# Kernel optimization log

Hardware: AMD Instinct MI355X
Metric: run time of the kernel (lower is better)

## Reference

```python
import jax, jax.numpy as jnp
import numpy as np

NEG_INF = -1e9  # matches masked_fill value -1000000000.0
SLOPE = 0.2     # LeakyReLU negative slope


def setup_inputs() -> dict:
    key = jax.random.key(0)
    k1, k2, k3, k4 = jax.random.split(key, 4)
    B, N, Fin, Fout = 16, 1024, 256, 256
    h = jax.random.normal(k1, (B, N, Fin), dtype=jnp.float32)
    adj = jax.random.randint(k2, (B, N, N), 0, 2, dtype=jnp.int32)
    W = jax.random.normal(k3, (Fin, Fout), dtype=jnp.float32) * (1.0 / np.sqrt(Fin))
    a = jax.random.normal(k4, (2 * Fout,), dtype=jnp.float32) * (1.0 / np.sqrt(2 * Fout))
    return {"h": h, "adj": adj, "W": W, "a": a}


def reference(h, adj, W, a):
    # h: [B,N,Fin], adj: [B,N,N] (0/1), W: [Fin,Fout], a: [2*Fout]
    Fout = W.shape[1]
    Wh = jnp.einsum("bnf,fo->bno", h, W)            # [B,N,Fout]
    a1, a2 = a[:Fout], a[Fout:]
    # e[b,i,j] = leakyrelu( Wh[b,i]·a1 + Wh[b,j]·a2 )  == a(cat(Wh_i, Wh_j))
    f1 = Wh @ a1                                     # [B,N]
    f2 = Wh @ a2                                     # [B,N]
    e = jax.nn.leaky_relu(f1[:, :, None] + f2[:, None, :], negative_slope=SLOPE)
    e = jnp.where(adj == 0, NEG_INF, e)              # mask non-edges
    attention = jax.nn.softmax(e, axis=-1)           # [B,N,N]
    # dropout is identity at eval / p=0
    h_prime = jnp.einsum("bij,bjo->bio", attention, Wh)  # [B,N,Fout]
    return h_prime
```

## Files before the change

kernel.cpp:

```cpp
#include <hip/hip_runtime.h>

typedef __attribute__((ext_vector_type(8))) short bf16x8;
typedef __attribute__((ext_vector_type(4))) float f32x4;

__device__ __forceinline__ unsigned short f2bf(float x) {
    unsigned int u = __float_as_uint(x);
    u += 0x7FFFu + ((u >> 16) & 1u);
    return (unsigned short)(u >> 16);
}

__device__ __forceinline__ void gl_lds16(const void* g, void* l) {
    __builtin_amdgcn_global_load_lds(
        (__attribute__((address_space(1))) void*)((void*)g),
        (__attribute__((address_space(3))) void*)l, 16, 0, 0);
}

__global__ __launch_bounds__(256) void prep(const float* __restrict__ W,
                                            short* __restrict__ WbT) {
    __shared__ float tile[32][33];
    const int t = threadIdx.x;
    const int bx = blockIdx.x & 7, by = blockIdx.x >> 3;
    const int r0 = by * 32, c0 = bx * 32;
    const int lr = t >> 5, lc = t & 31;
#pragma unroll
    for (int q = 0; q < 4; ++q)
        tile[q * 8 + lr][lc] = W[(r0 + q * 8 + lr) * 256 + c0 + lc];
    __syncthreads();
#pragma unroll
    for (int q = 0; q < 4; ++q)
        WbT[(c0 + q * 8 + lr) * 256 + r0 + lc] = (short)f2bf(tile[lc][q * 8 + lr]);
}

__global__ __launch_bounds__(256, 4) void wh_f12(const float* __restrict__ h,
                                                 const short* __restrict__ WbT,
                                                 const float* __restrict__ a,
                                                 short* __restrict__ WhT,
                                                 float* __restrict__ f1,
                                                 float* __restrict__ f2) {
    __shared__ short hA[32][264];
    __shared__ float sp[2][4][32];
    const int t = threadIdx.x;
    const int wid = t >> 6, lane = t & 63;
    const int quad = lane >> 4, l15 = lane & 15;
    const int m0 = blockIdx.x * 32;

#pragma unroll
    for (int rr = 0; rr < 2; ++rr) {
        const int r = rr * 16 + (t >> 4), c0 = (t & 15) * 16;
        const float* hp = h + (size_t)(m0 + r) * 256 + c0;
        float4 v0 = *(const float4*)(hp + 0), v1 = *(const float4*)(hp + 4);
        float4 v2 = *(const float4*)(hp + 8), v3 = *(const float4*)(hp + 12);
        bf16x8 w0, w1;
        w0[0] = (short)f2bf(v0.x); w0[1] = (short)f2bf(v0.y);
        w0[2] = (short)f2bf(v0.z); w0[3] = (short)f2bf(v0.w);
        w0[4] = (short)f2bf(v1.x); w0[5] = (short)f2bf(v1.y);
        w0[6] = (short)f2bf(v1.z); w0[7] = (short)f2bf(v1.w);
        w1[0] = (short)f2bf(v2.x); w1[1] = (short)f2bf(v2.y);
        w1[2] = (short)f2bf(v2.z); w1[3] = (short)f2bf(v2.w);
        w1[4] = (short)f2bf(v3.x); w1[5] = (short)f2bf(v3.y);
        w1[6] = (short)f2bf(v3.z); w1[7] = (short)f2bf(v3.w);
        *(bf16x8*)&hA[r][c0] = w0;
        *(bf16x8*)&hA[r][c0 + 8] = w1;
    }
    __syncthreads();

    f32x4 acc[2][4] = {};
#pragma unroll
    for (int kt = 0; kt < 8; ++kt) {
        const int k0 = kt * 32;
        bf16x8 bv[4];
#pragma unroll
        for (int ft = 0; ft < 4; ++ft)
            bv[ft] = *(const bf16x8*)(WbT + (size_t)(wid * 64 + ft * 16 + l15) * 256 + k0 + quad * 8);
        bf16x8 a0 = *(const bf16x8*)&hA[l15][k0 + quad * 8];
        bf16x8 a1 = *(const bf16x8*)&hA[16 + l15][k0 + quad * 8];
#pragma unroll
        for (int ft = 0; ft < 4; ++ft) {
            acc[0][ft] = __builtin_amdgcn_mfma_f32_16x16x32_bf16(a0, bv[ft], acc[0][ft], 0, 0, 0);
            acc[1][ft] = __builtin_amdgcn_mfma_f32_16x16x32_bf16(a1, bv[ft], acc[1][ft], 0, 0, 0);
        }
    }

    const int b = m0 >> 10;
#pragma unroll
    for (int mf = 0; mf < 2; ++mf) {
        const int il0 = (m0 & 1023) + mf * 16 + quad * 4;
#pragma unroll
        for (int ft = 0; ft < 4; ++ft) {
            const int f = wid * 64 + ft * 16 + l15;
            ushort4 pk;
            pk.x = f2bf(acc[mf][ft][0]);
            pk.y = f2bf(acc[mf][ft][1]);
            pk.z = f2bf(acc[mf][ft][2]);
            pk.w = f2bf(acc[mf][ft][3]);
            *(ushort4*)(WhT + ((size_t)b << 18) + (size_t)f * 1024 + il0) = pk;
        }
    }

    float a1v[4], a2v[4];
#pragma unroll
    for (int ft = 0; ft < 4; ++ft) {
        a1v[ft] = a[wid * 64 + ft * 16 + l15];
        a2v[ft] = a[256 + wid * 64 + ft * 16 + l15];
    }
    float p1[2][4] = {}, p2[2][4] = {};
#pragma unroll
    for (int mf = 0; mf < 2; ++mf)
#pragma unroll
        for (int ft = 0; ft < 4; ++ft)
#pragma unroll
            for (int r = 0; r < 4; ++r) {
                p1[mf][r] += acc[mf][ft][r] * a1v[ft];
                p2[mf][r] += acc[mf][ft][r] * a2v[ft];
            }
#pragma unroll
    for (int off = 1; off < 16; off <<= 1)
#pragma unroll
        for (int mf = 0; mf < 2; ++mf)
#pragma unroll
            for (int r = 0; r < 4; ++r) {
                p1[mf][r] += __shfl_xor(p1[mf][r], off);
                p2[mf][r] += __shfl_xor(p2[mf][r], off);
            }
    if (l15 == 0)
#pragma unroll
        for (int mf = 0; mf < 2; ++mf)
#pragma unroll
            for (int r = 0; r < 4; ++r) {
                sp[0][wid][mf * 16 + quad * 4 + r] = p1[mf][r];
                sp[1][wid][mf * 16 + quad * 4 + r] = p2[mf][r];
            }
    __syncthreads();
    if (t < 32) {
        f1[m0 + t] = sp[0][0][t] + sp[0][1][t] + sp[0][2][t] + sp[0][3][t];
        f2[m0 + t] = sp[1][0][t] + sp[1][1][t] + sp[1][2][t] + sp[1][3][t];
    }
}

__global__ __launch_bounds__(256, 2) void fused_agg(const int* __restrict__ adj,
                                                    const float* __restrict__ f1g,
                                                    const float* __restrict__ f2g,
                                                    const short* __restrict__ WhT,
                                                    float* __restrict__ out) {
    __shared__ short Ps[32 * 64];
    __shared__ short Bs[256 * 64];
    __shared__ float lred[256];
    __shared__ float linv[32];

    const int t = threadIdx.x;
    const int wid = t >> 6, lane = t & 63;
    const int quad = lane >> 4, l15 = lane & 15;

    const int id = blockIdx.x;
    const int xcd = id & 7, rest = id >> 3;
    const int b = xcd + 8 * (rest & 1);
    const int m0 = (rest >> 1) * 32;

    const int r = t >> 3, jc = t & 7;
    const float f1r = f1g[(b << 10) + m0 + r];
    const int* arow = adj + ((size_t)b << 20) + (size_t)(m0 + r) * 1024 + jc * 8;
    const float* f2p = f2g + (b << 10) + jc * 8;
    short* psw = Ps + r * 64 + (size_t)((jc ^ (r & 7)) * 8);

    const short* Wb = WhT + ((size_t)b << 18);
    const int rq0 = t >> 3, wB = (t & 7) ^ (rq0 & 7);
    const short* gB = Wb + (size_t)rq0 * 1024 + wB * 8;
    short* lB = Bs + t * 8;

    const int nq = wid * 64;
    f32x4 acc[2][4] = {};
    float lacc = 0.f;

    for (int k0 = 0; k0 < 1024; k0 += 64) {
#pragma unroll
        for (int q = 0; q < 8; ++q)
            gl_lds16(gB + k0 + q * 32768, lB + q * 2048);

        int4 a0 = *(const int4*)(arow + k0);
        int4 a1 = *(const int4*)(arow + k0 + 4);
        float4 w0 = *(const float4*)(f2p + k0);
        float4 w1 = *(const float4*)(f2p + k0 + 4);
        float xs[8] = {w0.x, w0.y, w0.z, w0.w, w1.x, w1.y, w1.z, w1.w};
        int ms[8] = {a0.x, a0.y, a0.z, a0.w, a1.x, a1.y, a1.z, a1.w};
        float pv[8];
#pragma unroll
        for (int u = 0; u < 8; ++u) {
            float x = f1r + xs[u];
            x = fmaxf(x, 0.2f * x);
            pv[u] = ms[u] ? __expf(x) : 0.f;
            lacc += pv[u];
        }
        bf16x8 pw;
#pragma unroll
        for (int u = 0; u < 8; ++u) pw[u] = (short)f2bf(pv[u]);
        *(bf16x8*)psw = pw;
        __syncthreads();

#pragma unroll
        for (int kt = 0; kt < 2; ++kt) {
            const int w = kt * 4 + quad;
            bf16x8 av[2], bv[4];
#pragma unroll
            for (int mf = 0; mf < 2; ++mf) {
                const int ra = mf * 16 + l15;
                av[mf] = *(const bf16x8*)(Ps + ra * 64 + ((w ^ (ra & 7)) * 8));
            }
#pragma unroll
            for (int nf = 0; nf < 4; ++nf) {
                const int rb = nq + nf * 16 + l15;
                bv[nf] = *(const bf16x8*)(Bs + rb * 64 + ((w ^ (rb & 7)) * 8));
            }
#pragma unroll
            for (int mf = 0; mf < 2; ++mf)
#pragma unroll
                for (int nf = 0; nf < 4; ++nf)
                    acc[mf][nf] = __builtin_amdgcn_mfma_f32_16x16x32_bf16(av[mf], bv[nf], acc[mf][nf], 0, 0, 0);
        }
        __syncthreads();
    }

    lred[t] = lacc;
    __syncthreads();
    if (t < 32) {
        const float* lp = lred + t * 8;
        linv[t] = 1.0f / (((lp[0] + lp[1]) + (lp[2] + lp[3])) +
                          ((lp[4] + lp[5]) + (lp[6] + lp[7])));
    }
    __syncthreads();

#pragma unroll
    for (int mf = 0; mf < 2; ++mf) {
        const int il = mf * 16 + quad * 4;
        const float i0 = linv[il], i1 = linv[il + 1];
        const float i2 = linv[il + 2], i3 = linv[il + 3];
#pragma unroll
        for (int nf = 0; nf < 4; ++nf) {
            float* op = out + (size_t)((b << 10) + m0 + il) * 256 + nq + nf * 16 + l15;
            op[0]   = acc[mf][nf][0] * i0;
            op[256] = acc[mf][nf][1] * i1;
            op[512] = acc[mf][nf][2] * i2;
            op[768] = acc[mf][nf][3] * i3;
        }
    }
}

extern "C" void kernel_launch(void* const* d_in, const int* in_sizes, int n_in,
                              void* d_out, int out_size, void* d_ws, size_t ws_size,
                              hipStream_t stream) {
    const float* h   = (const float*)d_in[0];
    const int*   adj = (const int*)d_in[1];
    const float* W   = (const float*)d_in[2];
    const float* a   = (const float*)d_in[3];
    float* out = (float*)d_out;

    short* WbT = (short*)d_ws;
    float* f1  = (float*)(WbT + 65536);
    float* f2  = f1 + 16384;
    short* WhT = (short*)(f2 + 16384);

    prep<<<64, 256, 0, stream>>>(W, WbT);
    wh_f12<<<512, 256, 0, stream>>>(h, WbT, a, WhT, f1, f2);
    fused_agg<<<512, 256, 0, stream>>>(adj, f1, f2, WhT, out);
}
```

Baseline: 148.0 us.

## Double-buffer LDS tiles to prefetch next adjacency and Wh tiles during MFMA

Doubles the P and B shared-memory tiles and restructures the K loop into a software pipeline. The global-to-LDS load of the next Wh tile and the adjacency/f2 loads for the next step are issued before the current MFMA block, and the next attention probabilities are computed after it. This removes one barrier per iteration and aims to hide global latency behind matrix math. In exchange LDS use roughly doubles to about 72KB per block, which may reduce how many blocks fit per CU under launch_bounds(256,2).

```diff
diff --git a/kernel.cpp b/kernel.cpp
--- a/kernel.cpp
+++ b/kernel.cpp
@@ -142,8 +142,8 @@
                                                     const float* __restrict__ f2g,
                                                     const short* __restrict__ WhT,
                                                     float* __restrict__ out) {
-    __shared__ short Ps[32 * 64];
-    __shared__ short Bs[256 * 64];
+    __shared__ short Ps[2][32 * 64];
+    __shared__ short Bs[2][256 * 64];
     __shared__ float lred[256];
     __shared__ float linv[32];
 
@@ -160,41 +160,56 @@
     const float f1r = f1g[(b << 10) + m0 + r];
     const int* arow = adj + ((size_t)b << 20) + (size_t)(m0 + r) * 1024 + jc * 8;
     const float* f2p = f2g + (b << 10) + jc * 8;
-    short* psw = Ps + r * 64 + (size_t)((jc ^ (r & 7)) * 8);
+    const int pswo = r * 64 + ((jc ^ (r & 7)) * 8);
 
     const short* Wb = WhT + ((size_t)b << 18);
     const int rq0 = t >> 3, wB = (t & 7) ^ (rq0 & 7);
     const short* gB = Wb + (size_t)rq0 * 1024 + wB * 8;
-    short* lB = Bs + t * 8;
 
     const int nq = wid * 64;
     f32x4 acc[2][4] = {};
     float lacc = 0.f;
 
-    for (int k0 = 0; k0 < 1024; k0 += 64) {
-#pragma unroll
-        for (int q = 0; q < 8; ++q)
-            gl_lds16(gB + k0 + q * 32768, lB + q * 2048);
-
-        int4 a0 = *(const int4*)(arow + k0);
-        int4 a1 = *(const int4*)(arow + k0 + 4);
-        float4 w0 = *(const float4*)(f2p + k0);
-        float4 w1 = *(const float4*)(f2p + k0 + 4);
+#pragma unroll
+    for (int q = 0; q < 8; ++q)
+        gl_lds16(gB + q * 32768, &Bs[0][0] + t * 8 + q * 2048);
+    {
+        int4 a0 = *(const int4*)(arow);
+        int4 a1 = *(const int4*)(arow + 4);
+        float4 w0 = *(const float4*)(f2p);
+        float4 w1 = *(const float4*)(f2p + 4);
         float xs[8] = {w0.x, w0.y, w0.z, w0.w, w1.x, w1.y, w1.z, w1.w};
         int ms[8] = {a0.x, a0.y, a0.z, a0.w, a1.x, a1.y, a1.z, a1.w};
-        float pv[8];
+        bf16x8 pw;
 #pragma unroll
         for (int u = 0; u < 8; ++u) {
             float x = f1r + xs[u];
             x = fmaxf(x, 0.2f * x);
-            pv[u] = ms[u] ? __expf(x) : 0.f;
-            lacc += pv[u];
-        }
-        bf16x8 pw;
-#pragma unroll
-        for (int u = 0; u < 8; ++u) pw[u] = (short)f2bf(pv[u]);
-        *(bf16x8*)psw = pw;
-        __syncthreads();
+            float pv = ms[u] ? __expf(x) : 0.f;
+            lacc += pv;
+            pw[u] = (short)f2bf(pv);
+        }
+        *(bf16x8*)(&Ps[0][0] + pswo) = pw;
+    }
+    __syncthreads();
+
+    for (int tt = 0; tt < 16; ++tt) {
+        const int cur = tt & 1;
+        const short* PsC = &Ps[cur][0];
+        const short* BsC = &Bs[cur][0];
+
+        int4 na0, na1;
+        float4 nw0, nw1;
+        if (tt < 15) {
+            const int k1 = (tt + 1) * 64;
+#pragma unroll
+            for (int q = 0; q < 8; ++q)
+                gl_lds16(gB + k1 + q * 32768, &Bs[cur ^ 1][0] + t * 8 + q * 2048);
+            na0 = *(const int4*)(arow + k1);
+            na1 = *(const int4*)(arow + k1 + 4);
+            nw0 = *(const float4*)(f2p + k1);
+            nw1 = *(const float4*)(f2p + k1 + 4);
+        }
 
 #pragma unroll
         for (int kt = 0; kt < 2; ++kt) {
@@ -203,18 +218,33 @@
 #pragma unroll
             for (int mf = 0; mf < 2; ++mf) {
                 const int ra = mf * 16 + l15;
-                av[mf] = *(const bf16x8*)(Ps + ra * 64 + ((w ^ (ra & 7)) * 8));
+                av[mf] = *(const bf16x8*)(PsC + ra * 64 + ((w ^ (ra & 7)) * 8));
             }
 #pragma unroll
             for (int nf = 0; nf < 4; ++nf) {
                 const int rb = nq + nf * 16 + l15;
-                bv[nf] = *(const bf16x8*)(Bs + rb * 64 + ((w ^ (rb & 7)) * 8));
+                bv[nf] = *(const bf16x8*)(BsC + rb * 64 + ((w ^ (rb & 7)) * 8));
             }
 #pragma unroll
             for (int mf = 0; mf < 2; ++mf)
 #pragma unroll
                 for (int nf = 0; nf < 4; ++nf)
                     acc[mf][nf] = __builtin_amdgcn_mfma_f32_16x16x32_bf16(av[mf], bv[nf], acc[mf][nf], 0, 0, 0);
+        }
+
+        if (tt < 15) {
+            float xs[8] = {nw0.x, nw0.y, nw0.z, nw0.w, nw1.x, nw1.y, nw1.z, nw1.w};
+            int ms[8] = {na0.x, na0.y, na0.z, na0.w, na1.x, na1.y, na1.z, na1.w};
+            bf16x8 pw;
+#pragma unroll
+            for (int u = 0; u < 8; ++u) {
+                float x = f1r + xs[u];
+                x = fmaxf(x, 0.2f * x);
+                float pv = ms[u] ? __expf(x) : 0.f;
+                lacc += pv;
+                pw[u] = (short)f2bf(pv);
+            }
+            *(bf16x8*)(&Ps[cur ^ 1][0] + pswo) = pw;
         }
         __syncthreads();
     }
```

Result: slower. 152.7 us (+3.2%).

## Precompute full attention row tile in LDS and stream Wh directly from global

Applied to the files above, without the earlier changes.

The aggregation kernel now uses 512-thread blocks covering 64 rows. It first computes the full 64x1024 bf16 probability tile into LDS (128KB) with a single barrier, instead of interleaving P production and Wh tile staging per 64-wide K step. Wh B-fragments are then loaded directly from global/L2 into registers with double buffering, removing the global-to-LDS staging and the per-iteration barriers. The cost is heavy LDS use, which limits occupancy to one block per CU, and more global/L2 traffic for Wh because each wave fetches its B fragments itself.

```diff
diff --git a/kernel.cpp b/kernel.cpp
--- a/kernel.cpp
+++ b/kernel.cpp
@@ -7,12 +7,6 @@
     unsigned int u = __float_as_uint(x);
     u += 0x7FFFu + ((u >> 16) & 1u);
     return (unsigned short)(u >> 16);
-}
-
-__device__ __forceinline__ void gl_lds16(const void* g, void* l) {
-    __builtin_amdgcn_global_load_lds(
-        (__attribute__((address_space(1))) void*)((void*)g),
-        (__attribute__((address_space(3))) void*)l, 16, 0, 0);
 }
 
 __global__ __launch_bounds__(256) void prep(const float* __restrict__ W,
@@ -137,15 +131,14 @@
     }
 }
 
-__global__ __launch_bounds__(256, 2) void fused_agg(const int* __restrict__ adj,
+__global__ __launch_bounds__(512, 2) void fused_agg(const int* __restrict__ adj,
                                                     const float* __restrict__ f1g,
                                                     const float* __restrict__ f2g,
                                                     const short* __restrict__ WhT,
                                                     float* __restrict__ out) {
-    __shared__ short Ps[32 * 64];
-    __shared__ short Bs[256 * 64];
-    __shared__ float lred[256];
-    __shared__ float linv[32];
+    __shared__ short Ps[64 * 1024];
+    __shared__ float lred[512];
+    __shared__ float linv[64];
 
     const int t = threadIdx.x;
     const int wid = t >> 6, lane = t & 63;
@@ -154,74 +147,85 @@
     const int id = blockIdx.x;
     const int xcd = id & 7, rest = id >> 3;
     const int b = xcd + 8 * (rest & 1);
-    const int m0 = (rest >> 1) * 32;
+    const int m0 = (rest >> 1) * 64;
 
     const int r = t >> 3, jc = t & 7;
     const float f1r = f1g[(b << 10) + m0 + r];
     const int* arow = adj + ((size_t)b << 20) + (size_t)(m0 + r) * 1024 + jc * 8;
     const float* f2p = f2g + (b << 10) + jc * 8;
-    short* psw = Ps + r * 64 + (size_t)((jc ^ (r & 7)) * 8);
-
-    const short* Wb = WhT + ((size_t)b << 18);
-    const int rq0 = t >> 3, wB = (t & 7) ^ (rq0 & 7);
-    const short* gB = Wb + (size_t)rq0 * 1024 + wB * 8;
-    short* lB = Bs + t * 8;
-
-    const int nq = wid * 64;
-    f32x4 acc[2][4] = {};
+    short* prow = Ps + r * 1024;
+    const int rx = r & 7;
     float lacc = 0.f;
-
-    for (int k0 = 0; k0 < 1024; k0 += 64) {
-#pragma unroll
-        for (int q = 0; q < 8; ++q)
-            gl_lds16(gB + k0 + q * 32768, lB + q * 2048);
-
-        int4 a0 = *(const int4*)(arow + k0);
-        int4 a1 = *(const int4*)(arow + k0 + 4);
-        float4 w0 = *(const float4*)(f2p + k0);
-        float4 w1 = *(const float4*)(f2p + k0 + 4);
+#pragma unroll 4
+    for (int i = 0; i < 16; ++i) {
+        int4 a0 = *(const int4*)(arow + i * 64);
+        int4 a1 = *(const int4*)(arow + i * 64 + 4);
+        float4 w0 = *(const float4*)(f2p + i * 64);
+        float4 w1 = *(const float4*)(f2p + i * 64 + 4);
         float xs[8] = {w0.x, w0.y, w0.z, w0.w, w1.x, w1.y, w1.z, w1.w};
         int ms[8] = {a0.x, a0.y, a0.z, a0.w, a1.x, a1.y, a1.z, a1.w};
-        float pv[8];
+        bf16x8 pw;
 #pragma unroll
         for (int u = 0; u < 8; ++u) {
             float x = f1r + xs[u];
             x = fmaxf(x, 0.2f * x);
-            pv[u] = ms[u] ? __expf(x) : 0.f;
-            lacc += pv[u];
-        }
-        bf16x8 pw;
-#pragma unroll
-        for (int u = 0; u < 8; ++u) pw[u] = (short)f2bf(pv[u]);
-        *(bf16x8*)psw = pw;
-        __syncthreads();
-
+            float pv = ms[u] ? __expf(x) : 0.f;
+            lacc += pv;
+            pw[u] = (short)f2bf(pv);
+        }
+        *(bf16x8*)(prow + (((i * 8 + jc) ^ rx) * 8)) = pw;
+    }
+    lred[t] = lacc;
+    __syncthreads();
+
+    const int wm = wid >> 2, wn = wid & 3;
+    const int mh = wm * 32, nq = wn * 64;
+    const short* Wb = WhT + ((size_t)b << 18);
+    const short* pB0 = Wb + (size_t)(nq + l15) * 1024 + quad * 8;
+    const short* pB1 = pB0 + 16 * 1024;
+    const short* pB2 = pB0 + 32 * 1024;
+    const short* pB3 = pB0 + 48 * 1024;
+    const short* rowA0 = Ps + (size_t)(mh + l15) * 1024;
+    const short* rowA1 = rowA0 + 16 * 1024;
+    const int sx = l15 & 7;
+
+    f32x4 acc[2][4] = {};
+    bf16x8 bA[8], bB[8];
+
+    auto loadB = [&](bf16x8* dst, int T) {
 #pragma unroll
         for (int kt = 0; kt < 2; ++kt) {
-            const int w = kt * 4 + quad;
-            bf16x8 av[2], bv[4];
-#pragma unroll
-            for (int mf = 0; mf < 2; ++mf) {
-                const int ra = mf * 16 + l15;
-                av[mf] = *(const bf16x8*)(Ps + ra * 64 + ((w ^ (ra & 7)) * 8));
-            }
+            dst[kt * 4 + 0] = *(const bf16x8*)(pB0 + T * 64 + kt * 32);
+            dst[kt * 4 + 1] = *(const bf16x8*)(pB1 + T * 64 + kt * 32);
+            dst[kt * 4 + 2] = *(const bf16x8*)(pB2 + T * 64 + kt * 32);
+            dst[kt * 4 + 3] = *(const bf16x8*)(pB3 + T * 64 + kt * 32);
+        }
+    };
+    auto tile = [&](bf16x8* bv, int T) {
+#pragma unroll
+        for (int kt = 0; kt < 2; ++kt) {
+            const int sw = ((T * 8 + kt * 4 + quad) ^ sx) * 8;
+            bf16x8 av0 = *(const bf16x8*)(rowA0 + sw);
+            bf16x8 av1 = *(const bf16x8*)(rowA1 + sw);
 #pragma unroll
             for (int nf = 0; nf < 4; ++nf) {
-                const int rb = nq + nf * 16 + l15;
-                bv[nf] = *(const bf16x8*)(Bs + rb * 64 + ((w ^ (rb & 7)) * 8));
-            }
-#pragma unroll
-            for (int mf = 0; mf < 2; ++mf)
-#pragma unroll
-                for (int nf = 0; nf < 4; ++nf)
-                    acc[mf][nf] = __builtin_amdgcn_mfma_f32_16x16x32_bf16(av[mf], bv[nf], acc[mf][nf], 0, 0, 0);
-        }
-        __syncthreads();
-    }
-
-    lred[t] = lacc;
-    __syncthreads();
-    if (t < 32) {
+                acc[0][nf] = __builtin_amdgcn_mfma_f32_16x16x32_bf16(av0, bv[kt * 4 + nf], acc[0][nf], 0, 0, 0);
+                acc[1][nf] = __builtin_amdgcn_mfma_f32_16x16x32_bf16(av1, bv[kt * 4 + nf], acc[1][nf], 0, 0, 0);
+            }
+        }
+    };
+
+    loadB(bA, 0);
+#pragma unroll
+    for (int tp = 0; tp < 8; ++tp) {
+        const int t0 = tp * 2, t1 = t0 + 1;
+        loadB(bB, t1);
+        tile(bA, t0);
+        if (t1 < 15) loadB(bA, t1 + 1);
+        tile(bB, t1);
+    }
+
+    if (t < 64) {
         const float* lp = lred + t * 8;
         linv[t] = 1.0f / (((lp[0] + lp[1]) + (lp[2] + lp[3])) +
                           ((lp[4] + lp[5]) + (lp[6] + lp[7])));
@@ -230,7 +234,7 @@
 
 #pragma unroll
     for (int mf = 0; mf < 2; ++mf) {
-        const int il = mf * 16 + quad * 4;
+        const int il = mh + mf * 16 + quad * 4;
         const float i0 = linv[il], i1 = linv[il + 1];
         const float i2 = linv[il + 2], i3 = linv[il + 3];
 #pragma unroll
@@ -260,5 +264,5 @@
 
     prep<<<64, 256, 0, stream>>>(W, WbT);
     wh_f12<<<512, 256, 0, stream>>>(h, WbT, a, WhT, f1, f2);
-    fused_agg<<<512, 256, 0, stream>>>(adj, f1, f2, WhT, out);
-}
+    fused_agg<<<256, 512, 0, stream>>>(adj, f1, f2, WhT, out);
+}
```

Result: slower. 154.5 us (+4.4%).

## Bitpack adjacency, enlarge agg tiles, and triple-buffer WhT staging

Applied to the files above, without the earlier changes.

Adds a separate kernel that packs the int32 adjacency mask into 64-bit bitmasks with wave ballots. The aggregation kernel then reads the bits from LDS instead of streaming int32 adjacency. The aggregation kernel now uses 512-thread blocks covering 64 rows each, halving redundant WhT loads per output row. It also triple-buffers the WhT tiles and double-buffers the P tiles, with explicit waitcnt and barriers so loads and P generation overlap the MFMAs. The extra bitpack pass still reads all of adj once, and the larger LDS footprint may limit occupancy.

```diff
diff --git a/kernel.cpp b/kernel.cpp
--- a/kernel.cpp
+++ b/kernel.cpp
@@ -14,6 +14,8 @@
         (__attribute__((address_space(1))) void*)((void*)g),
         (__attribute__((address_space(3))) void*)l, 16, 0, 0);
 }
+
+#define SFENCE __builtin_amdgcn_sched_barrier(0)
 
 __global__ __launch_bounds__(256) void prep(const float* __restrict__ W,
                                             short* __restrict__ WbT) {
@@ -29,6 +31,21 @@
 #pragma unroll
     for (int q = 0; q < 4; ++q)
         WbT[(c0 + q * 8 + lr) * 256 + r0 + lc] = (short)f2bf(tile[lc][q * 8 + lr]);
+}
+
+__global__ __launch_bounds__(256) void bitpack(const int* __restrict__ adj,
+                                               unsigned long long* __restrict__ bits) {
+    const int wid = threadIdx.x >> 6, lane = threadIdx.x & 63;
+    const int row = blockIdx.x * 4 + wid;
+    const int* arow = adj + (size_t)row * 1024;
+    unsigned long long myword = 0ull;
+#pragma unroll
+    for (int w = 0; w < 16; ++w) {
+        int v = arow[w * 64 + lane];
+        unsigned long long bal = __ballot(v != 0);
+        if (lane == w) myword = bal;
+    }
+    if (lane < 16) bits[(size_t)row * 16 + lane] = myword;
 }
 
 __global__ __launch_bounds__(256, 4) void wh_f12(const float* __restrict__ h,
@@ -137,15 +154,17 @@
     }
 }
 
-__global__ __launch_bounds__(256, 2) void fused_agg(const int* __restrict__ adj,
+__global__ __launch_bounds__(512, 2) void fused_agg(const unsigned long long* __restrict__ bitsG,
                                                     const float* __restrict__ f1g,
                                                     const float* __restrict__ f2g,
                                                     const short* __restrict__ WhT,
                                                     float* __restrict__ out) {
-    __shared__ short Ps[32 * 64];
-    __shared__ short Bs[256 * 64];
-    __shared__ float lred[256];
-    __shared__ float linv[32];
+    __shared__ short Bs[3][256 * 64];
+    __shared__ short Ps[2][64 * 64];
+    __shared__ unsigned long long bitsS[16 * 64];
+    __shared__ float f2s[1024];
+    __shared__ float lred[512];
+    __shared__ float linv[64];
 
     const int t = threadIdx.x;
     const int wid = t >> 6, lane = t & 63;
@@ -154,61 +173,68 @@
     const int id = blockIdx.x;
     const int xcd = id & 7, rest = id >> 3;
     const int b = xcd + 8 * (rest & 1);
-    const int m0 = (rest >> 1) * 32;
-
-    const int r = t >> 3, jc = t & 7;
-    const float f1r = f1g[(b << 10) + m0 + r];
-    const int* arow = adj + ((size_t)b << 20) + (size_t)(m0 + r) * 1024 + jc * 8;
-    const float* f2p = f2g + (b << 10) + jc * 8;
-    short* psw = Ps + r * 64 + (size_t)((jc ^ (r & 7)) * 8);
+    const int m0 = (rest >> 1) * 64;
 
     const short* Wb = WhT + ((size_t)b << 18);
-    const int rq0 = t >> 3, wB = (t & 7) ^ (rq0 & 7);
-    const short* gB = Wb + (size_t)rq0 * 1024 + wB * 8;
-    short* lB = Bs + t * 8;
-
-    const int nq = wid * 64;
+
+    {
+        const unsigned long long* bsrc = bitsG + (size_t)((b << 10) + m0) * 16;
+        ulonglong2 bv = ((const ulonglong2*)bsrc)[t];
+        const int g0 = 2 * t, g1 = 2 * t + 1;
+        bitsS[(g0 & 15) * 64 + (g0 >> 4)] = bv.x;
+        bitsS[(g1 & 15) * 64 + (g1 >> 4)] = bv.y;
+        ((float2*)f2s)[t] = ((const float2*)(f2g + (b << 10)))[t];
+    }
+    const int pr = t >> 3, ps = t & 7;
+    const float f1r = f1g[(b << 10) + m0 + pr];
+    __syncthreads();
+
+    auto stage = [&](int T, short* buf) {
+#pragma unroll
+        for (int q = 0; q < 4; ++q) {
+            const int c = t + 512 * q;
+            const int rr = c >> 3;
+            const int sl = (c & 7) ^ (rr & 7);
+            gl_lds16(Wb + (size_t)rr * 1024 + T * 64 + sl * 8, buf + c * 8);
+        }
+    };
+
+    float lacc = 0.f;
+    auto pgen = [&](int T, short* pbuf) {
+        unsigned int m8 = (unsigned int)(bitsS[T * 64 + pr] >> (ps * 8)) & 0xffu;
+        float4 fa = *(const float4*)(f2s + T * 64 + ps * 8);
+        float4 fb = *(const float4*)(f2s + T * 64 + ps * 8 + 4);
+        float xv[8] = {fa.x, fa.y, fa.z, fa.w, fb.x, fb.y, fb.z, fb.w};
+        bf16x8 pw;
+#pragma unroll
+        for (int u = 0; u < 8; ++u) {
+            float x = f1r + xv[u];
+            x = fmaxf(x, 0.2f * x);
+            float pv = ((m8 >> u) & 1u) ? __expf(x) : 0.f;
+            lacc += pv;
+            pw[u] = (short)f2bf(pv);
+        }
+        *(bf16x8*)(pbuf + pr * 64 + ((ps ^ (pr & 7)) * 8)) = pw;
+    };
+
+    const int wm = wid >> 2, wn = wid & 3;
+    const int mh = wm * 32, nq = wn * 64;
     f32x4 acc[2][4] = {};
-    float lacc = 0.f;
-
-    for (int k0 = 0; k0 < 1024; k0 += 64) {
-#pragma unroll
-        for (int q = 0; q < 8; ++q)
-            gl_lds16(gB + k0 + q * 32768, lB + q * 2048);
-
-        int4 a0 = *(const int4*)(arow + k0);
-        int4 a1 = *(const int4*)(arow + k0 + 4);
-        float4 w0 = *(const float4*)(f2p + k0);
-        float4 w1 = *(const float4*)(f2p + k0 + 4);
-        float xs[8] = {w0.x, w0.y, w0.z, w0.w, w1.x, w1.y, w1.z, w1.w};
-        int ms[8] = {a0.x, a0.y, a0.z, a0.w, a1.x, a1.y, a1.z, a1.w};
-        float pv[8];
-#pragma unroll
-        for (int u = 0; u < 8; ++u) {
-            float x = f1r + xs[u];
-            x = fmaxf(x, 0.2f * x);
-            pv[u] = ms[u] ? __expf(x) : 0.f;
-            lacc += pv[u];
-        }
-        bf16x8 pw;
-#pragma unroll
-        for (int u = 0; u < 8; ++u) pw[u] = (short)f2bf(pv[u]);
-        *(bf16x8*)psw = pw;
-        __syncthreads();
-
+
+    auto step = [&](const short* pbuf, const short* bbuf) {
 #pragma unroll
         for (int kt = 0; kt < 2; ++kt) {
             const int w = kt * 4 + quad;
             bf16x8 av[2], bv[4];
 #pragma unroll
             for (int mf = 0; mf < 2; ++mf) {
-                const int ra = mf * 16 + l15;
-                av[mf] = *(const bf16x8*)(Ps + ra * 64 + ((w ^ (ra & 7)) * 8));
+                const int ra = mh + mf * 16 + l15;
+                av[mf] = *(const bf16x8*)(pbuf + ra * 64 + ((w ^ (ra & 7)) * 8));
             }
 #pragma unroll
             for (int nf = 0; nf < 4; ++nf) {
                 const int rb = nq + nf * 16 + l15;
-                bv[nf] = *(const bf16x8*)(Bs + rb * 64 + ((w ^ (rb & 7)) * 8));
+                bv[nf] = *(const bf16x8*)(bbuf + rb * 64 + ((w ^ (rb & 7)) * 8));
             }
 #pragma unroll
             for (int mf = 0; mf < 2; ++mf)
@@ -216,12 +242,40 @@
                 for (int nf = 0; nf < 4; ++nf)
                     acc[mf][nf] = __builtin_amdgcn_mfma_f32_16x16x32_bf16(av[mf], bv[nf], acc[mf][nf], 0, 0, 0);
         }
-        __syncthreads();
+    };
+
+    stage(0, Bs[0]);
+    stage(1, Bs[1]);
+    pgen(0, Ps[0]);
+    asm volatile("s_waitcnt lgkmcnt(0)" ::: "memory");
+    SFENCE;
+    asm volatile("s_waitcnt vmcnt(4)" ::: "memory");
+    SFENCE;
+    __builtin_amdgcn_s_barrier();
+    SFENCE;
+
+#pragma unroll
+    for (int T = 0; T < 16; ++T) {
+        if (T < 15) pgen(T + 1, Ps[(T + 1) & 1]);
+        step(Ps[T & 1], Bs[T % 3]);
+        asm volatile("s_waitcnt lgkmcnt(0)" ::: "memory");
+        SFENCE;
+        __builtin_amdgcn_s_barrier();
+        SFENCE;
+        if (T < 14) {
+            stage(T + 2, Bs[(T + 2) % 3]);
+            asm volatile("s_waitcnt vmcnt(4)" ::: "memory");
+        } else {
+            asm volatile("s_waitcnt vmcnt(0)" ::: "memory");
+        }
+        SFENCE;
+        __builtin_amdgcn_s_barrier();
+        SFENCE;
     }
 
     lred[t] = lacc;
     __syncthreads();
-    if (t < 32) {
+    if (t < 64) {
         const float* lp = lred + t * 8;
         linv[t] = 1.0f / (((lp[0] + lp[1]) + (lp[2] + lp[3])) +
                           ((lp[4] + lp[5]) + (lp[6] + lp[7])));
@@ -230,7 +284,7 @@
 
 #pragma unroll
     for (int mf = 0; mf < 2; ++mf) {
-        const int il = mf * 16 + quad * 4;
+        const int il = mh + mf * 16 + quad * 4;
         const float i0 = linv[il], i1 = linv[il + 1];
         const float i2 = linv[il + 2], i3 = linv[il + 3];
 #pragma unroll
@@ -257,8 +311,11 @@
     float* f1  = (float*)(WbT + 65536);
     float* f2  = f1 + 16384;
     short* WhT = (short*)(f2 + 16384);
+    unsigned long long* bits =
+        (unsigned long long*)(WhT + 16 * 256 * 1024);
 
     prep<<<64, 256, 0, stream>>>(W, WbT);
+    bitpack<<<4096, 256, 0, stream>>>(adj, bits);
     wh_f12<<<512, 256, 0, stream>>>(h, WbT, a, WhT, f1, f2);
-    fused_agg<<<512, 256, 0, stream>>>(adj, f1, f2, WhT, out);
-}
+    fused_agg<<<256, 512, 0, stream>>>(bits, f1, f2, WhT, out);
+}
```

Measured after the change: 141.3 us. 1.05x faster.
